# Kernel optimization log

Hardware: AMD Instinct MI355X
Metric: run time of the kernel (lower is better)

## Reference

```python
import jax, jax.numpy as jnp
import numpy as np
from jax import lax

BN_EPS = 1e-5


def conv_bn_relu(x, W, g, b, m, v):
    # 3x3 conv, pad=1, stride=1, no bias; then inference-mode BN; then ReLU
    y = lax.conv_general_dilated(x, W, (1, 1), 'SAME',
                                 dimension_numbers=('NCHW', 'OIHW', 'NCHW'))
    scale = g / jnp.sqrt(v + BN_EPS)
    y = y * scale[None, :, None, None] + (b - m * scale)[None, :, None, None]
    return jax.nn.relu(y)


def shifted_windows(y, d, pad_val):
    # y: [n,c,h,w] -> [k*k, n, c, h, w] of all spatial shifts within radius d
    n, c, h, w = y.shape
    yp = jnp.pad(y, ((0, 0), (0, 0), (d, d), (d, d)), constant_values=pad_val)
    k = 2 * d + 1
    return jnp.stack([yp[:, :, i:i + h, j:j + w] for i in range(k) for j in range(k)], axis=0)


def setup_inputs() -> dict:
    key = jax.random.key(0)
    ks = jax.random.split(key, 16)
    n_clip, n, C_in, H, W = 2, 2, 512, 64, 64
    emb_dim, fc_dim, num_class = 256, 128, 124

    def bn_params(k, c):
        k1, k2, k3, k4 = jax.random.split(k, 4)
        return (jax.random.uniform(k1, (c,)) + 0.5,
                jax.random.normal(k2, (c,)) * 0.1,
                jax.random.normal(k3, (c,)) * 0.1,
                jax.random.uniform(k4, (c,)) + 0.5)

    emb_g, emb_b, emb_m, emb_v = bn_params(ks[0], emb_dim)
    emb2_g, emb2_b, emb2_m, emb2_v = bn_params(ks[1], fc_dim)
    return {
        'clip_embs': jax.random.normal(ks[2], (n_clip * n, C_in, H, W), dtype=jnp.float32),
        'clip_num': 2,
        'emb_W': jax.random.normal(ks[3], (emb_dim, C_in, 3, 3), dtype=jnp.float32) * 0.02,
        'emb_g': emb_g, 'emb_b': emb_b, 'emb_m': emb_m, 'emb_v': emb_v,
        'emb2_W': jax.random.normal(ks[4], (fc_dim, C_in, 3, 3), dtype=jnp.float32) * 0.02,
        'emb2_g': emb2_g, 'emb2_b': emb2_b, 'emb2_m': emb2_m, 'emb2_v': emb2_v,
        'last_W': jax.random.normal(ks[5], (num_class, emb_dim, 1, 1), dtype=jnp.float32) * 0.05,
        'last_b': jnp.zeros((num_class,), dtype=jnp.float32),
    }


MAX_DISTANCES = (2,)
TEMP = 1.0


def reference(clip_embs, clip_num, emb_W, emb_g, emb_b, emb_m, emb_v,
              emb2_W, emb2_g, emb2_b, emb2_m, emb2_v, last_W, last_b):
    # emb_2 features used for the local cost volume (fc_dim channels)
    clip_emb2 = conv_bn_relu(clip_embs, emb2_W, emb2_g, emb2_b, emb2_m, emb2_v)
    chunks2 = jnp.split(clip_emb2, clip_num, axis=0)
    c2 = chunks2[-1]                      # current frame, [n, fc_dim, h, w]
    others2 = chunks2[:-1]

    x2 = jnp.sum(c2 * c2, axis=1)         # [n,h,w]

    all_weights = []                       # per other clip: per max_distance softmax weights
    for other in others2:
        y2 = jnp.sum(other * other, axis=1, keepdims=True)  # [n,1,h,w]
        w_list = []
        for d in MAX_DISTANCES:
            k = 2 * d + 1
            y_sh = shifted_windows(other, d, 0.0)            # [k2,n,c,h,w]
            y2_sh = shifted_windows(y2, d, 1e20)[:, :, 0]    # [k2,n,h,w]
            cross = jnp.einsum('nchw,onchw->onhw', c2, y_sh)
            dist = x2[None] + y2_sh - 2.0 * cross            # [k2,n,h,w] squared L2
            # distsoftmax branch: softmax over the k*k window of 1/(dist*temp+1e-5)
            w_ = jax.nn.softmax(1.0 / (dist * TEMP + 1e-5), axis=0)
            w_list.append(w_)
        all_weights.append(w_list)

    # emb features (emb_dim channels) that get warped
    clip_emb_s = conv_bn_relu(clip_embs, emb_W, emb_g, emb_b, emb_m, emb_v)
    chunks_s = jnp.split(clip_emb_s, clip_num, axis=0)
    c_img = chunks_s[-1]                   # [n, emb_dim, h, w]
    others_s = chunks_s[:-1]

    final_emb = [c_img]
    for other, w_list in zip(others_s, all_weights):
        warp_fs = []
        for d, w_ in zip(MAX_DISTANCES, w_list):
            k = 2 * d + 1
            o_sh = shifted_windows(other, d, 0.0)            # [k2,n,c,h,w]
            # weighted sum over window, then avgpool over k*k -> divide by k*k
            warp = jnp.einsum('onchw,onhw->nchw', o_sh, w_) / (k * k)
            warp_fs.append(warp)
        final_emb.append(jnp.mean(jnp.stack(warp_fs, axis=-1), axis=-1))

    # linear_combine=False: mean over the clip embeddings
    final_fea = jnp.mean(jnp.stack(final_emb, axis=-1), axis=-1)

    # last_layer: dropout (eval -> identity) + 1x1 conv
    logits = jnp.einsum('nchw,oc->nohw', final_fea, last_W[:, :, 0, 0]) + last_b[None, :, None, None]
    x = jax.nn.log_softmax(logits, axis=1)
    return (x, clip_emb2)
```

## Files before the change

### kernel.cpp

```cpp
#include <hip/hip_runtime.h>
#include <hip/hip_bf16.h>
#include <stdint.h>


typedef float v4f __attribute__((ext_vector_type(4)));
typedef __bf16 v8bf __attribute__((ext_vector_type(8)));
typedef unsigned short u16;
typedef unsigned int u32;
typedef u16 u16x8 __attribute__((ext_vector_type(8)));

constexpr size_t XH_OFF  = 0;
constexpr size_t XH_BYTES = (size_t)4*66*66*512*2;
constexpr size_t WT_OFF  = XH_OFF + XH_BYTES;
constexpr size_t WT_BYTES = (size_t)9*384*512*2;
constexpr size_t FS_OFF  = WT_OFF + WT_BYTES;
constexpr size_t FS_BYTES = (size_t)4*68*68*256*2;
constexpr size_t F2_OFF  = FS_OFF + FS_BYTES;
constexpr size_t F2_BYTES = (size_t)4*68*68*128*4;
constexpr size_t Y2_OFF  = F2_OFF + F2_BYTES;
constexpr size_t Y2_BYTES = (size_t)2*68*68*4;
constexpr size_t FEA_OFF = Y2_OFF + Y2_BYTES;
constexpr size_t FEA_BYTES = (size_t)2*4096*256*2;
constexpr size_t WL_OFF  = FEA_OFF + FEA_BYTES;
constexpr size_t WL_BYTES = (size_t)128*256*2;
constexpr size_t SC_OFF  = WL_OFF + WL_BYTES;
constexpr size_t WS_TOTAL = SC_OFF + 768*4;

__device__ __forceinline__ float bf2f(u16 h) { return __uint_as_float(((u32)h) << 16); }
__device__ __forceinline__ u16 f2bf(float f) {
  u32 u = __float_as_uint(f);
  return (u16)((u + 0x7fffu + ((u >> 16) & 1u)) >> 16);
}

__device__ __forceinline__ void gld16(const void* g, const void* l) {
  __builtin_amdgcn_global_load_lds(
      (const __attribute__((address_space(1))) void*)(uintptr_t)g,
      (__attribute__((address_space(3))) void*)(u32)(uintptr_t)l,
      16, 0, 0);
}

__global__ void k_init(const float* __restrict__ eg, const float* __restrict__ eb,
                       const float* __restrict__ em, const float* __restrict__ ev,
                       const float* __restrict__ e2g, const float* __restrict__ e2b,
                       const float* __restrict__ e2m, const float* __restrict__ e2v,
                       const float* __restrict__ lw,
                       u16* __restrict__ Xh, u16* __restrict__ Fs, float* __restrict__ F2,
                       float* __restrict__ Y2, u16* __restrict__ Wl,
                       float* __restrict__ sc, float* __restrict__ bi) {
  const u32 N0 = 4u * 260u * 64u;
  const u32 N1 = 4u * 528u * 32u;
  const u32 N2 = 4u * 528u * 32u;
  const u32 N3 = 2u * 68u * 68u;
  const u32 N4 = 4096u;
  const u32 N5 = 384u;
  const u32 TOT = N0 + N1 + N2 + N3 + N4 + N5;
  const u16x8 z8 = {0,0,0,0,0,0,0,0};
  for (u32 i = blockIdx.x * 256u + threadIdx.x; i < TOT; i += gridDim.x * 256u) {
    if (i < N0) {
      const u32 img = i / (260u * 64u);
      const u32 rem = i - img * (260u * 64u);
      const u32 r = rem >> 6, ch8 = rem & 63u;
      u32 prow, pcol;
      if (r < 132u) { prow = (r >= 66u) ? 65u : 0u; pcol = r - ((r >= 66u) ? 66u : 0u); }
      else { const u32 rr = r - 132u; prow = 1u + (rr >> 1); pcol = (rr & 1u) * 65u; }
      *(u16x8*)(Xh + ((size_t)((img * 66u + prow) * 66u + pcol)) * 512u + ch8 * 8u) = z8;
    } else if (i < N0 + N1 + N2) {
      const bool isF2 = (i >= N0 + N1);
      const u32 j = isF2 ? (i - N0 - N1) : (i - N0);
      const u32 img = j / (528u * 32u);
      const u32 rem = j - img * (528u * 32u);
      const u32 r = rem >> 5, cg = rem & 31u;
      u32 prow, pcol;
      if (r < 272u) { const u32 q = r / 68u; prow = (q < 2u) ? q : q + 64u; pcol = r - q * 68u; }
      else { const u32 rr = r - 272u; prow = 2u + (rr >> 2); const u32 c = rr & 3u; pcol = (c < 2u) ? c : c + 64u; }
      if (isF2) {
        const float4 zf = {0.f, 0.f, 0.f, 0.f};
        *(float4*)(F2 + ((size_t)((img * 68u + prow) * 68u + pcol)) * 128u + cg * 4u) = zf;
      } else {
        *(u16x8*)(Fs + ((size_t)((img * 68u + prow) * 68u + pcol)) * 256u + cg * 8u) = z8;
      }
    } else if (i < N0 + N1 + N2 + N3) {
      const u32 j = i - N0 - N1 - N2;
      const u32 n = j / 4624u, rc = j - n * 4624u;
      const u32 rr = rc / 68u, cc = rc - rr * 68u;
      const bool interior = (rr >= 2u && rr < 66u && cc >= 2u && cc < 66u);
      Y2[j] = interior ? 0.f : 1e20f;
    } else if (i < N0 + N1 + N2 + N3 + N4) {
      const u32 j = i - N0 - N1 - N2 - N3;
      const u32 row = j >> 5, c8 = (j & 31u) * 8u;
      u16x8 o;
      #pragma unroll
      for (int k = 0; k < 8; ++k) o[k] = (row < 124u) ? f2bf(lw[row * 256u + c8 + k]) : (u16)0;
      *(u16x8*)(Wl + (size_t)row * 256u + c8) = o;
    } else {
      const u32 id = i - N0 - N1 - N2 - N3 - N4;
      float g, b, m, v;
      if (id < 256u) { g = eg[id]; b = eb[id]; m = em[id]; v = ev[id]; }
      else { const u32 q = id - 256u; g = e2g[q]; b = e2b[q]; m = e2m[q]; v = e2v[q]; }
      const float s = g / sqrtf(v + 1e-5f);
      sc[id] = s;
      bi[id] = b - m * s;
    }
  }
}

__global__ __launch_bounds__(256) void k_prep_x(const float* __restrict__ X, u16* __restrict__ Xh) {
  __shared__ __align__(16) float tile[64 * 65];
  const int tid = threadIdx.x;
  const int n = blockIdx.x >> 7;
  const int rem = blockIdx.x & 127;
  const int h = rem >> 1, chalf = rem & 1;
  const int wq = tid >> 6, wcol = tid & 63;
  #pragma unroll 1
  for (int it = 0; it < 4; ++it) {
    const int c0 = chalf * 256 + it * 64;
    __syncthreads();
    #pragma unroll
    for (int i = 0; i < 16; ++i) {
      const int cl = i * 4 + wq;
      tile[cl * 65 + wcol] = X[((size_t)(n * 512 + c0 + cl)) * 4096 + h * 64 + wcol];
    }
    __syncthreads();
    const int w = tid >> 2, cg = tid & 3;
    u16x8 a, b;
    #pragma unroll
    for (int j = 0; j < 8; ++j) a[j] = f2bf(tile[(cg * 16 + j) * 65 + w]);
    #pragma unroll
    for (int j = 0; j < 8; ++j) b[j] = f2bf(tile[(cg * 16 + 8 + j) * 65 + w]);
    u16* dst = Xh + ((size_t)((n * 66 + h + 1) * 66 + (w + 1))) * 512 + c0 + cg * 16;
    *(u16x8*)dst = a;
    *((u16x8*)dst + 1) = b;
  }
}

__global__ __launch_bounds__(256) void k_prep_w(const float* __restrict__ embW, const float* __restrict__ emb2W,
                                                u16* __restrict__ Wt) {
  __shared__ float row[4608];
  const int oc = blockIdx.x;
  const int tid = threadIdx.x;
  const float* src = (oc < 256) ? (embW + (size_t)oc * 4608) : (emb2W + (size_t)(oc - 256) * 4608);
  for (int i = tid; i < 4608; i += 256) row[i] = src[i];
  __syncthreads();
  #pragma unroll
  for (int pos = 0; pos < 9; ++pos) {
    const u32 pk = (u32)f2bf(row[(2 * tid) * 9 + pos]) | ((u32)f2bf(row[(2 * tid + 1) * 9 + pos]) << 16);
    *(u32*)(Wt + ((size_t)(pos * 384 + oc)) * 512 + 2 * tid) = pk;
  }
}

__global__ __launch_bounds__(256) void k_conv(const u16* __restrict__ Xh, const u16* __restrict__ Wt,
                                              const float* __restrict__ sc, const float* __restrict__ bi,
                                              float* __restrict__ out2, float* __restrict__ F2,
                                              u16* __restrict__ Fs, float* __restrict__ Y2) {
  __shared__ __align__(16) char lds[42496];
  const int tid = threadIdx.x;
  const int wvi = tid >> 6, lane = tid & 63;
  const int octile = blockIdx.x >> 7;
  const int rest = blockIdx.x & 127;
  const int n = rest >> 5, pt = rest & 31;
  const int h0 = pt * 2;
  const int oc0 = octile * 64;
  const int pxrow = wvi >> 1;
  const int pxc0 = (wvi & 1) * 32;

  float* scl = (float*)(lds + 41984);
  float* bil = scl + 64;
  if (tid < 64) { scl[tid] = sc[oc0 + tid]; bil[tid] = bi[oc0 + tid]; }

  const int arow = tid >> 2;
  const size_t asrc0 = (size_t)(oc0 + arow) * 512 + (((tid & 3) ^ (arow & 3)) << 3);
  const u16* xbase = Xh + (size_t)n * 66 * 66 * 512;
  int bofs[5];
  #pragma unroll
  for (int k = 0; k < 5; ++k) {
    const int idx = k * 256 + tid;
    if (idx < 1056) {
      const int col = idx >> 2;
      const int ssrc = (idx & 3) ^ (col & 3);
      const int imgrow = col / 66, c = col - imgrow * 66;
      bofs[k] = ((h0 + imgrow) * 66 + c) * 512 + ssrc * 8;
    } else bofs[k] = 0;
  }

  auto stageA = [&](int pos, int cc, int buf) {
    gld16(Wt + (size_t)pos * 384 * 512 + asrc0 + cc * 32, lds + buf * 4096 + wvi * 1024);
  };
  auto stageB = [&](int cc, int buf) {
    char* base = lds + 8192 + buf * 16896;
    #pragma unroll
    for (int k = 0; k < 4; ++k)
      gld16(xbase + bofs[k] + cc * 32, base + k * 4096 + wvi * 1024);
    if (tid < 32) gld16(xbase + bofs[4] + cc * 32, base + 16384);
  };

  v4f acc[4][2];
  #pragma unroll
  for (int mt = 0; mt < 4; ++mt) { acc[mt][0] = (v4f){0,0,0,0}; acc[mt][1] = (v4f){0,0,0,0}; }

  int bA = 0, bB = 0;
  stageB(0, 0);
  stageA(0, 0, 0);
  __syncthreads();

  #pragma unroll 1
  for (int cc = 0; cc < 16; ++cc) {
    #pragma unroll
    for (int pos = 0; pos < 9; ++pos) {
      const int ky = pos / 3, kx = pos % 3;
      if (pos < 8) {
        stageA(pos + 1, cc, bA ^ 1);
      } else if (cc < 15) {
        stageB(cc + 1, bB ^ 1);
        stageA(0, cc + 1, bA ^ 1);
      }
      v8bf af[4], bfr[2];
      const char* pA = lds + bA * 4096 + ((lane & 15) << 6) + ((((lane >> 4) ^ (lane & 3))) << 4);
      #pragma unroll
      for (int mt = 0; mt < 4; ++mt) af[mt] = *(const v8bf*)(pA + mt * 1024);
      #pragma unroll
      for (int nt = 0; nt < 2; ++nt) {
        const int rb = (pxrow + ky) * 66 + pxc0 + nt * 16 + (lane & 15) + kx;
        bfr[nt] = *(const v8bf*)(lds + 8192 + bB * 16896 + (rb << 6) + (((lane >> 4) ^ (rb & 3)) << 4));
      }
      #pragma unroll
      for (int mt = 0; mt < 4; ++mt)
        #pragma unroll
        for (int nt = 0; nt < 2; ++nt)
          acc[mt][nt] = __builtin_amdgcn_mfma_f32_16x16x32_bf16(af[mt], bfr[nt], acc[mt][nt], 0, 0, 0);
      __syncthreads();
      bA ^= 1;
      if (pos == 8) bB ^= 1;
    }
  }

  float vals[4][2][4];
  #pragma unroll
  for (int mt = 0; mt < 4; ++mt) {
    const int ocb = mt * 16 + ((lane >> 4) << 2);
    #pragma unroll
    for (int j = 0; j < 4; ++j) {
      const float s = scl[ocb + j], tt = bil[ocb + j];
      #pragma unroll
      for (int nt = 0; nt < 2; ++nt) vals[mt][nt][j] = fmaxf(fmaf(acc[mt][nt][j], s, tt), 0.f);
    }
  }

  if (octile >= 4) {
    #pragma unroll
    for (int mt = 0; mt < 4; ++mt)
      #pragma unroll
      for (int j = 0; j < 4; ++j) {
        const int oc = (octile - 4) * 64 + mt * 16 + ((lane >> 4) << 2) + j;
        float* orow = out2 + ((size_t)(n * 128 + oc)) * 4096 + (h0 + pxrow) * 64 + pxc0;
        orow[(lane & 15)] = vals[mt][0][j];
        orow[16 + (lane & 15)] = vals[mt][1][j];
      }
    if (n < 2) {
      #pragma unroll
      for (int nt = 0; nt < 2; ++nt) {
        float s = 0.f;
        #pragma unroll
        for (int mt = 0; mt < 4; ++mt)
          #pragma unroll
          for (int j = 0; j < 4; ++j) s = fmaf(vals[mt][nt][j], vals[mt][nt][j], s);
        s += __shfl_xor(s, 16);
        s += __shfl_xor(s, 32);
        if ((lane >> 4) == 0)
          atomicAdd(&Y2[(size_t)(n * 68 + h0 + pxrow + 2) * 68 + pxc0 + nt * 16 + (lane & 15) + 2], s);
      }
    }
    float* T = (float*)lds;
    #pragma unroll
    for (int mt = 0; mt < 4; ++mt)
      #pragma unroll
      for (int nt = 0; nt < 2; ++nt)
        #pragma unroll
        for (int j = 0; j < 4; ++j)
          T[(wvi * 32 + nt * 16 + (lane & 15)) * 64 + mt * 16 + ((lane >> 4) << 2) + j] = vals[mt][nt][j];
    __syncthreads();
    const int px = tid >> 1, half = tid & 1;
    const float4* Tp = (const float4*)(T + px * 64 + half * 32);
    float4* dst = (float4*)(F2 + ((size_t)((n * 68 + h0 + (px >> 6) + 2) * 68 + (px & 63) + 2)) * 128 + (octile - 4) * 64 + half * 32);
    #pragma unroll
    for (int i = 0; i < 8; ++i) dst[i] = Tp[i];
  } else {
    u16* T = (u16*)lds;
    #pragma unroll
    for (int mt = 0; mt < 4; ++mt)
      #pragma unroll
      for (int nt = 0; nt < 2; ++nt)
        #pragma unroll
        for (int jj = 0; jj < 2; ++jj) {
          const u32 pk = (u32)f2bf(vals[mt][nt][2 * jj]) | ((u32)f2bf(vals[mt][nt][2 * jj + 1]) << 16);
          *(u32*)(T + (wvi * 32 + nt * 16 + (lane & 15)) * 64 + mt * 16 + ((lane >> 4) << 2) + 2 * jj) = pk;
        }
    __syncthreads();
    const int px = tid >> 1, half = tid & 1;
    const u16x8* Tp = (const u16x8*)(T + px * 64 + half * 32);
    u16x8* dst = (u16x8*)(Fs + ((size_t)((n * 68 + h0 + (px >> 6) + 2) * 68 + (px & 63) + 2)) * 256 + octile * 64 + half * 32);
    #pragma unroll
    for (int i = 0; i < 4; ++i) dst[i] = Tp[i];
  }
}

__global__ __launch_bounds__(256) void k_dw(const float* __restrict__ F2, const float* __restrict__ Y2,
                                            const u16* __restrict__ Fs, u16* __restrict__ Fea) {
  const int t = blockIdx.x * 256 + threadIdx.x;
  const int g = t & 7;
  const int px = t >> 3;
  const int n = px >> 12;
  const int p = px & 4095;
  const int h = p >> 6, w = p & 63;

  const float4* c2p = (const float4*)(F2 + ((size_t)(((n + 2) * 68 + h + 2) * 68 + (w + 2))) * 128 + g * 16);
  float4 c2v[4];
  float x2 = 0.f;
  #pragma unroll
  for (int i = 0; i < 4; ++i) {
    c2v[i] = c2p[i];
    x2 += c2v[i].x * c2v[i].x + c2v[i].y * c2v[i].y + c2v[i].z * c2v[i].z + c2v[i].w * c2v[i].w;
  }
  float cross[25];
  #pragma unroll
  for (int dy = 0; dy < 5; ++dy) {
    const float* rowp = F2 + ((size_t)((n * 68 + h + dy) * 68 + w)) * 128 + g * 16;
    #pragma unroll
    for (int dx = 0; dx < 5; ++dx) {
      const float4* wp = (const float4*)(rowp + dx * 128);
      float s = 0.f;
      #pragma unroll
      for (int i = 0; i < 4; ++i) {
        const float4 u = wp[i];
        s += c2v[i].x * u.x + c2v[i].y * u.y + c2v[i].z * u.z + c2v[i].w * u.w;
      }
      cross[dy * 5 + dx] = s;
    }
  }
  x2 += __shfl_xor(x2, 1); x2 += __shfl_xor(x2, 2); x2 += __shfl_xor(x2, 4);
  #pragma unroll
  for (int o = 0; o < 25; ++o) {
    cross[o] += __shfl_xor(cross[o], 1);
    cross[o] += __shfl_xor(cross[o], 2);
    cross[o] += __shfl_xor(cross[o], 4);
  }
  float wv[25], mx = -1e30f;
  #pragma unroll
  for (int dy = 0; dy < 5; ++dy)
    #pragma unroll
    for (int dx = 0; dx < 5; ++dx) {
      const int o = dy * 5 + dx;
      const float y2v = Y2[(size_t)(n * 68 + h + dy) * 68 + (w + dx)];
      const float dist = x2 + y2v - 2.f * cross[o];
      const float l = 1.f / (dist + 1e-5f);
      wv[o] = l;
      mx = fmaxf(mx, l);
    }
  float ssum = 0.f;
  #pragma unroll
  for (int o = 0; o < 25; ++o) { const float e = __expf(wv[o] - mx); wv[o] = e; ssum += e; }
  const float inv = 1.f / ssum;
  #pragma unroll
  for (int o = 0; o < 25; ++o) wv[o] *= inv;

  float facc[32];
  #pragma unroll
  for (int i = 0; i < 32; ++i) facc[i] = 0.f;
  #pragma unroll
  for (int dy = 0; dy < 5; ++dy) {
    const u16* rp = Fs + ((size_t)((n * 68 + h + dy) * 68 + w)) * 256 + g * 32;
    #pragma unroll
    for (int dx = 0; dx < 5; ++dx) {
      const float wt = wv[dy * 5 + dx];
      const u16x8* up = (const u16x8*)(rp + dx * 256);
      #pragma unroll
      for (int k = 0; k < 4; ++k) {
        const u16x8 u = up[k];
        #pragma unroll
        for (int j = 0; j < 8; ++j) facc[k * 8 + j] = fmaf(wt, bf2f(u[j]), facc[k * 8 + j]);
      }
    }
  }
  const u16x8* cip = (const u16x8*)(Fs + ((size_t)(((n + 2) * 68 + h + 2) * 68 + (w + 2))) * 256 + g * 32);
  u16x8* dp = (u16x8*)(Fea + ((size_t)(n * 4096 + p)) * 256 + g * 32);
  #pragma unroll
  for (int k = 0; k < 4; ++k) {
    const u16x8 cu = cip[k];
    u16x8 ou;
    #pragma unroll
    for (int j = 0; j < 8; ++j)
      ou[j] = f2bf(0.5f * (bf2f(cu[j]) + facc[k * 8 + j] * (1.f / 25.f)));
    dp[k] = ou;
  }
}

__global__ __launch_bounds__(128) void k_logits(const u16* __restrict__ Fea, const u16* __restrict__ Wl,
                                                const float* __restrict__ lb, float* __restrict__ xout) {
  const int wvi = threadIdx.x >> 6, lane = threadIdx.x & 63;
  const int wid = blockIdx.x * 2 + wvi;
  const int n = wid >> 8;
  const int p0 = (wid & 255) * 16;
  const int lp = lane & 15;
  const int kb = (lane >> 4) * 8;

  v4f acc[8];
  #pragma unroll
  for (int mt = 0; mt < 8; ++mt) acc[mt] = (v4f){0.f, 0.f, 0.f, 0.f};

  #pragma unroll
  for (int kc = 0; kc < 8; ++kc) {
    const v8bf b = *(const v8bf*)(Fea + ((size_t)(n * 4096 + p0 + lp)) * 256 + kc * 32 + kb);
    #pragma unroll
    for (int mt = 0; mt < 8; ++mt) {
      const v8bf a = *(const v8bf*)(Wl + ((size_t)(mt * 16 + lp)) * 256 + kc * 32 + kb);
      acc[mt] = __builtin_amdgcn_mfma_f32_16x16x32_bf16(a, b, acc[mt], 0, 0, 0);
    }
  }
  const int r0 = (lane >> 4) * 4;
  float v[8][4];
  float mx = -1e30f;
  #pragma unroll
  for (int mt = 0; mt < 8; ++mt)
    #pragma unroll
    for (int j = 0; j < 4; ++j) {
      const int cls = mt * 16 + r0 + j;
      const float val = (cls < 124) ? (acc[mt][j] + lb[cls]) : -1e30f;
      v[mt][j] = val;
      mx = fmaxf(mx, val);
    }
  mx = fmaxf(mx, __shfl_xor(mx, 16));
  mx = fmaxf(mx, __shfl_xor(mx, 32));
  float s = 0.f;
  #pragma unroll
  for (int mt = 0; mt < 8; ++mt)
    #pragma unroll
    for (int j = 0; j < 4; ++j) {
      const int cls = mt * 16 + r0 + j;
      if (cls < 124) s += __expf(v[mt][j] - mx);
    }
  s += __shfl_xor(s, 16);
  s += __shfl_xor(s, 32);
  const float lz = mx + logf(s);
  #pragma unroll
  for (int mt = 0; mt < 8; ++mt)
    #pragma unroll
    for (int j = 0; j < 4; ++j) {
      const int cls = mt * 16 + r0 + j;
      if (cls < 124)
        xout[((size_t)(n * 124 + cls)) * 4096 + p0 + lp] = v[mt][j] - lz;
    }
}

extern "C" void kernel_launch(void* const* d_in, const int* in_sizes, int n_in,
                              void* d_out, int out_size, void* d_ws, size_t ws_size,
                              hipStream_t stream) {
  (void)in_sizes; (void)n_in; (void)out_size;
  const float* clip  = (const float*)d_in[0];
  const float* embW  = (const float*)d_in[2];
  const float* eg    = (const float*)d_in[3];
  const float* eb    = (const float*)d_in[4];
  const float* em    = (const float*)d_in[5];
  const float* ev    = (const float*)d_in[6];
  const float* emb2W = (const float*)d_in[7];
  const float* e2g   = (const float*)d_in[8];
  const float* e2b   = (const float*)d_in[9];
  const float* e2m   = (const float*)d_in[10];
  const float* e2v   = (const float*)d_in[11];
  const float* lw    = (const float*)d_in[12];
  const float* lb    = (const float*)d_in[13];

  char* ws = (char*)d_ws;
  u16*   Xh  = (u16*)(ws + XH_OFF);
  u16*   Wt  = (u16*)(ws + WT_OFF);
  u16*   Fs  = (u16*)(ws + FS_OFF);
  float* F2  = (float*)(ws + F2_OFF);
  float* Y2  = (float*)(ws + Y2_OFF);
  u16*   Fea = (u16*)(ws + FEA_OFF);
  u16*   Wl  = (u16*)(ws + WL_OFF);
  float* sc  = (float*)(ws + SC_OFF);
  float* bi  = sc + 384;

  float* xout = (float*)d_out;
  float* out2 = xout + (size_t)2 * 124 * 64 * 64;

  if (ws_size < WS_TOTAL) return;

  k_init<<<256, 256, 0, stream>>>(eg, eb, em, ev, e2g, e2b, e2m, e2v, lw, Xh, Fs, F2, Y2, Wl, sc, bi);
  k_prep_x<<<512, 256, 0, stream>>>(clip, Xh);
  k_prep_w<<<384, 256, 0, stream>>>(embW, emb2W, Wt);
  k_conv<<<768, 256, 0, stream>>>(Xh, Wt, sc, bi, out2, F2, Fs, Y2);
  k_dw<<<256, 256, 0, stream>>>(F2, Y2, Fs, Fea);
  k_logits<<<256, 128, 0, stream>>>(Fea, Wl, lb, xout);
}
```

Baseline: 207.7 us.

## Enlarge conv tile to 128 channels with register-direct fragment-layout weights

Weights are pre-packed into an MFMA fragment layout so each wave loads its A operands straight from global memory into registers, prefetched one tap ahead. This removes the A staging through LDS and the per-tap barrier. Each block now computes 128 output channels by 128 pixels, halving the block count and reusing each staged input tile across twice as many channels. The input tile is swizzled differently and the epilogue is reworked. The depthwise warp kernel is also split across twice as many threads with narrower channel groups. In exchange the block uses more accumulator registers and has fewer blocks to hide latency.

Result: slower. 221.5 us (+6.6%).

```diff
diff --git a/kernel.cpp b/kernel.cpp
--- a/kernel.cpp
+++ b/kernel.cpp
@@ -12,7 +12,7 @@
 constexpr size_t XH_OFF  = 0;
 constexpr size_t XH_BYTES = (size_t)4*66*66*512*2;
 constexpr size_t WT_OFF  = XH_OFF + XH_BYTES;
-constexpr size_t WT_BYTES = (size_t)9*384*512*2;
+constexpr size_t WT_BYTES = (size_t)9*16*24*64*8*2;
 constexpr size_t FS_OFF  = WT_OFF + WT_BYTES;
 constexpr size_t FS_BYTES = (size_t)4*68*68*256*2;
 constexpr size_t F2_OFF  = FS_OFF + FS_BYTES;
@@ -134,41 +134,41 @@
 }
 
 __global__ __launch_bounds__(256) void k_prep_w(const float* __restrict__ embW, const float* __restrict__ emb2W,
-                                                u16* __restrict__ Wt) {
+                                                u16* __restrict__ Wf) {
   __shared__ float row[4608];
   const int oc = blockIdx.x;
   const int tid = threadIdx.x;
   const float* src = (oc < 256) ? (embW + (size_t)oc * 4608) : (emb2W + (size_t)(oc - 256) * 4608);
   for (int i = tid; i < 4608; i += 256) row[i] = src[i];
   __syncthreads();
+  const int cc = tid >> 4;
+  const int slot = (tid >> 2) & 3;
+  const int e = 2 * (tid & 3);
+  const int r = oc & 15, ocb = oc >> 4;
   #pragma unroll
   for (int pos = 0; pos < 9; ++pos) {
     const u32 pk = (u32)f2bf(row[(2 * tid) * 9 + pos]) | ((u32)f2bf(row[(2 * tid + 1) * 9 + pos]) << 16);
-    *(u32*)(Wt + ((size_t)(pos * 384 + oc)) * 512 + 2 * tid) = pk;
-  }
-}
-
-__global__ __launch_bounds__(256) void k_conv(const u16* __restrict__ Xh, const u16* __restrict__ Wt,
+    *(u32*)(Wf + ((size_t)((pos * 16 + cc) * 24 + ocb)) * 512 + (slot * 16 + r) * 8 + e) = pk;
+  }
+}
+
+__global__ __launch_bounds__(256) void k_conv(const u16* __restrict__ Xh, const u16* __restrict__ Wf,
                                               const float* __restrict__ sc, const float* __restrict__ bi,
                                               float* __restrict__ out2, float* __restrict__ F2,
                                               u16* __restrict__ Fs, float* __restrict__ Y2) {
-  __shared__ __align__(16) char lds[42496];
+  __shared__ __align__(16) char lds[34816];
   const int tid = threadIdx.x;
   const int wvi = tid >> 6, lane = tid & 63;
   const int octile = blockIdx.x >> 7;
   const int rest = blockIdx.x & 127;
   const int n = rest >> 5, pt = rest & 31;
   const int h0 = pt * 2;
-  const int oc0 = octile * 64;
-  const int pxrow = wvi >> 1;
-  const int pxc0 = (wvi & 1) * 32;
-
-  float* scl = (float*)(lds + 41984);
-  float* bil = scl + 64;
-  if (tid < 64) { scl[tid] = sc[oc0 + tid]; bil[tid] = bi[oc0 + tid]; }
-
-  const int arow = tid >> 2;
-  const size_t asrc0 = (size_t)(oc0 + arow) * 512 + (((tid & 3) ^ (arow & 3)) << 3);
+  const int ochalf = wvi >> 1, prow = wvi & 1;
+
+  float* scl = (float*)(lds + 33792);
+  float* bil = scl + 128;
+  if (tid < 128) { scl[tid] = sc[octile * 128 + tid]; bil[tid] = bi[octile * 128 + tid]; }
+
   const u16* xbase = Xh + (size_t)n * 66 * 66 * 512;
   int bofs[5];
   #pragma unroll
@@ -176,30 +176,42 @@
     const int idx = k * 256 + tid;
     if (idx < 1056) {
       const int col = idx >> 2;
-      const int ssrc = (idx & 3) ^ (col & 3);
+      const int ssrc = (idx & 3) ^ ((col >> 1) & 3);
       const int imgrow = col / 66, c = col - imgrow * 66;
       bofs[k] = ((h0 + imgrow) * 66 + c) * 512 + ssrc * 8;
     } else bofs[k] = 0;
   }
 
-  auto stageA = [&](int pos, int cc, int buf) {
-    gld16(Wt + (size_t)pos * 384 * 512 + asrc0 + cc * 32, lds + buf * 4096 + wvi * 1024);
+  auto stageB = [&](int cc, int buf) {
+    char* base = lds + buf * 16896;
+    #pragma unroll
+    for (int k = 0; k < 4; ++k)
+      gld16(xbase + bofs[k] + cc * 32, base + k * 4096 + tid * 16);
+    if (tid < 32) gld16(xbase + bofs[4] + cc * 32, base + 16384 + tid * 16);
   };
-  auto stageB = [&](int cc, int buf) {
-    char* base = lds + 8192 + buf * 16896;
-    #pragma unroll
-    for (int k = 0; k < 4; ++k)
-      gld16(xbase + bofs[k] + cc * 32, base + k * 4096 + wvi * 1024);
-    if (tid < 32) gld16(xbase + bofs[4] + cc * 32, base + 16384);
+
+  const int ocb0 = octile * 8 + ochalf * 4;
+  const int lane8 = lane * 8;
+  auto loadA = [&](int pos, int cc, int mt) {
+    return *(const v8bf*)(Wf + ((size_t)((pos * 16 + cc) * 24 + ocb0 + mt)) * 512 + lane8);
   };
-
-  v4f acc[4][2];
-  #pragma unroll
-  for (int mt = 0; mt < 4; ++mt) { acc[mt][0] = (v4f){0,0,0,0}; acc[mt][1] = (v4f){0,0,0,0}; }
-
-  int bA = 0, bB = 0;
+  const int rbB = prow * 66 + (lane & 15);
+  const int slotb = lane >> 4;
+  auto readB = [&](int buf, int rb) {
+    return *(const v8bf*)(lds + buf * 16896 + rb * 64 + (((slotb ^ ((rb >> 1) & 3))) << 4));
+  };
+
+  v4f acc[4][4];
+  #pragma unroll
+  for (int mt = 0; mt < 4; ++mt)
+    #pragma unroll
+    for (int nt = 0; nt < 4; ++nt) acc[mt][nt] = (v4f){0.f, 0.f, 0.f, 0.f};
+
+  int buf = 0;
   stageB(0, 0);
-  stageA(0, 0, 0);
+  v8bf ac[4];
+  #pragma unroll
+  for (int mt = 0; mt < 4; ++mt) ac[mt] = loadA(0, 0, mt);
   __syncthreads();
 
   #pragma unroll 1
@@ -207,57 +219,58 @@
     #pragma unroll
     for (int pos = 0; pos < 9; ++pos) {
       const int ky = pos / 3, kx = pos % 3;
+      if (pos == 5 && cc < 15) stageB(cc + 1, buf ^ 1);
+      v8bf an[4];
       if (pos < 8) {
-        stageA(pos + 1, cc, bA ^ 1);
+        #pragma unroll
+        for (int mt = 0; mt < 4; ++mt) an[mt] = loadA(pos + 1, cc, mt);
       } else if (cc < 15) {
-        stageB(cc + 1, bB ^ 1);
-        stageA(0, cc + 1, bA ^ 1);
-      }
-      v8bf af[4], bfr[2];
-      const char* pA = lds + bA * 4096 + ((lane & 15) << 6) + ((((lane >> 4) ^ (lane & 3))) << 4);
-      #pragma unroll
-      for (int mt = 0; mt < 4; ++mt) af[mt] = *(const v8bf*)(pA + mt * 1024);
-      #pragma unroll
-      for (int nt = 0; nt < 2; ++nt) {
-        const int rb = (pxrow + ky) * 66 + pxc0 + nt * 16 + (lane & 15) + kx;
-        bfr[nt] = *(const v8bf*)(lds + 8192 + bB * 16896 + (rb << 6) + (((lane >> 4) ^ (rb & 3)) << 4));
-      }
+        #pragma unroll
+        for (int mt = 0; mt < 4; ++mt) an[mt] = loadA(0, cc + 1, mt);
+      } else {
+        #pragma unroll
+        for (int mt = 0; mt < 4; ++mt) an[mt] = ac[mt];
+      }
+      v8bf bfr[4];
+      #pragma unroll
+      for (int nt = 0; nt < 4; ++nt)
+        bfr[nt] = readB(buf, rbB + ky * 66 + kx + nt * 16);
       #pragma unroll
       for (int mt = 0; mt < 4; ++mt)
         #pragma unroll
-        for (int nt = 0; nt < 2; ++nt)
-          acc[mt][nt] = __builtin_amdgcn_mfma_f32_16x16x32_bf16(af[mt], bfr[nt], acc[mt][nt], 0, 0, 0);
-      __syncthreads();
-      bA ^= 1;
-      if (pos == 8) bB ^= 1;
-    }
-  }
-
-  float vals[4][2][4];
+        for (int nt = 0; nt < 4; ++nt)
+          acc[mt][nt] = __builtin_amdgcn_mfma_f32_16x16x32_bf16(ac[mt], bfr[nt], acc[mt][nt], 0, 0, 0);
+      if (pos == 8) { __syncthreads(); buf ^= 1; }
+      #pragma unroll
+      for (int mt = 0; mt < 4; ++mt) ac[mt] = an[mt];
+    }
+  }
+
+  float vals[4][4][4];
   #pragma unroll
   for (int mt = 0; mt < 4; ++mt) {
-    const int ocb = mt * 16 + ((lane >> 4) << 2);
+    const int ocb = ochalf * 64 + mt * 16 + ((lane >> 4) << 2);
     #pragma unroll
     for (int j = 0; j < 4; ++j) {
       const float s = scl[ocb + j], tt = bil[ocb + j];
       #pragma unroll
-      for (int nt = 0; nt < 2; ++nt) vals[mt][nt][j] = fmaxf(fmaf(acc[mt][nt][j], s, tt), 0.f);
-    }
-  }
-
-  if (octile >= 4) {
+      for (int nt = 0; nt < 4; ++nt) vals[mt][nt][j] = fmaxf(fmaf(acc[mt][nt][j], s, tt), 0.f);
+    }
+  }
+
+  if (octile == 2) {
     #pragma unroll
     for (int mt = 0; mt < 4; ++mt)
       #pragma unroll
       for (int j = 0; j < 4; ++j) {
-        const int oc = (octile - 4) * 64 + mt * 16 + ((lane >> 4) << 2) + j;
-        float* orow = out2 + ((size_t)(n * 128 + oc)) * 4096 + (h0 + pxrow) * 64 + pxc0;
-        orow[(lane & 15)] = vals[mt][0][j];
-        orow[16 + (lane & 15)] = vals[mt][1][j];
+        const int ocl = ochalf * 64 + mt * 16 + ((lane >> 4) << 2) + j;
+        float* orow = out2 + ((size_t)(n * 128 + ocl)) * 4096 + (h0 + prow) * 64;
+        #pragma unroll
+        for (int nt = 0; nt < 4; ++nt) orow[nt * 16 + (lane & 15)] = vals[mt][nt][j];
       }
     if (n < 2) {
       #pragma unroll
-      for (int nt = 0; nt < 2; ++nt) {
+      for (int nt = 0; nt < 4; ++nt) {
         float s = 0.f;
         #pragma unroll
         for (int mt = 0; mt < 4; ++mt)
@@ -266,82 +279,100 @@
         s += __shfl_xor(s, 16);
         s += __shfl_xor(s, 32);
         if ((lane >> 4) == 0)
-          atomicAdd(&Y2[(size_t)(n * 68 + h0 + pxrow + 2) * 68 + pxc0 + nt * 16 + (lane & 15) + 2], s);
+          atomicAdd(&Y2[(size_t)(n * 68 + h0 + prow + 2) * 68 + nt * 16 + (lane & 15) + 2], s);
       }
     }
     float* T = (float*)lds;
-    #pragma unroll
-    for (int mt = 0; mt < 4; ++mt)
-      #pragma unroll
-      for (int nt = 0; nt < 2; ++nt)
-        #pragma unroll
-        for (int j = 0; j < 4; ++j)
-          T[(wvi * 32 + nt * 16 + (lane & 15)) * 64 + mt * 16 + ((lane >> 4) << 2) + j] = vals[mt][nt][j];
-    __syncthreads();
-    const int px = tid >> 1, half = tid & 1;
-    const float4* Tp = (const float4*)(T + px * 64 + half * 32);
-    float4* dst = (float4*)(F2 + ((size_t)((n * 68 + h0 + (px >> 6) + 2) * 68 + (px & 63) + 2)) * 128 + (octile - 4) * 64 + half * 32);
-    #pragma unroll
-    for (int i = 0; i < 8; ++i) dst[i] = Tp[i];
+    #pragma unroll 1
+    for (int mr = 0; mr < 2; ++mr) {
+      __syncthreads();
+      if (ochalf == mr) {
+        #pragma unroll
+        for (int mt = 0; mt < 4; ++mt)
+          #pragma unroll
+          for (int nt = 0; nt < 4; ++nt) {
+            const int p = prow * 64 + nt * 16 + (lane & 15);
+            #pragma unroll
+            for (int j = 0; j < 4; ++j) {
+              const int c = mt * 16 + ((lane >> 4) << 2) + j;
+              T[p * 64 + (((c >> 2) ^ (p & 15)) << 2) + (c & 3)] = vals[mt][nt][j];
+            }
+          }
+      }
+      __syncthreads();
+      const int p = tid >> 1, half = tid & 1;
+      float* dst = F2 + ((size_t)((n * 68 + h0 + (p >> 6) + 2) * 68 + (p & 63) + 2)) * 128 + mr * 64 + half * 32;
+      #pragma unroll
+      for (int i = 0; i < 8; ++i) {
+        const int s = (half * 8 + i) ^ (p & 15);
+        *(float4*)(dst + i * 4) = *(const float4*)(T + p * 64 + s * 4);
+      }
+    }
   } else {
     u16* T = (u16*)lds;
     #pragma unroll
     for (int mt = 0; mt < 4; ++mt)
       #pragma unroll
-      for (int nt = 0; nt < 2; ++nt)
+      for (int nt = 0; nt < 4; ++nt) {
+        const int p = prow * 64 + nt * 16 + (lane & 15);
         #pragma unroll
         for (int jj = 0; jj < 2; ++jj) {
           const u32 pk = (u32)f2bf(vals[mt][nt][2 * jj]) | ((u32)f2bf(vals[mt][nt][2 * jj + 1]) << 16);
-          *(u32*)(T + (wvi * 32 + nt * 16 + (lane & 15)) * 64 + mt * 16 + ((lane >> 4) << 2) + 2 * jj) = pk;
+          const int c = ochalf * 64 + mt * 16 + ((lane >> 4) << 2) + 2 * jj;
+          *(u32*)(T + p * 128 + (((c >> 3) ^ (p & 15)) << 3) + (c & 7)) = pk;
         }
+      }
     __syncthreads();
-    const int px = tid >> 1, half = tid & 1;
-    const u16x8* Tp = (const u16x8*)(T + px * 64 + half * 32);
-    u16x8* dst = (u16x8*)(Fs + ((size_t)((n * 68 + h0 + (px >> 6) + 2) * 68 + (px & 63) + 2)) * 256 + octile * 64 + half * 32);
-    #pragma unroll
-    for (int i = 0; i < 4; ++i) dst[i] = Tp[i];
+    const int p = tid >> 1, half = tid & 1;
+    u16* dst = Fs + ((size_t)((n * 68 + h0 + (p >> 6) + 2) * 68 + (p & 63) + 2)) * 256 + octile * 128 + half * 64;
+    #pragma unroll
+    for (int i = 0; i < 8; ++i) {
+      const int s = (half * 8 + i) ^ (p & 15);
+      *(u16x8*)(dst + i * 8) = *(const u16x8*)(T + p * 128 + s * 8);
+    }
   }
 }
 
 __global__ __launch_bounds__(256) void k_dw(const float* __restrict__ F2, const float* __restrict__ Y2,
                                             const u16* __restrict__ Fs, u16* __restrict__ Fea) {
   const int t = blockIdx.x * 256 + threadIdx.x;
-  const int g = t & 7;
-  const int px = t >> 3;
+  const int g = t & 15;
+  const int px = t >> 4;
   const int n = px >> 12;
   const int p = px & 4095;
   const int h = p >> 6, w = p & 63;
 
-  const float4* c2p = (const float4*)(F2 + ((size_t)(((n + 2) * 68 + h + 2) * 68 + (w + 2))) * 128 + g * 16);
-  float4 c2v[4];
+  const float4* c2p = (const float4*)(F2 + ((size_t)(((n + 2) * 68 + h + 2) * 68 + (w + 2))) * 128 + g * 8);
+  float4 c2v[2];
   float x2 = 0.f;
   #pragma unroll
-  for (int i = 0; i < 4; ++i) {
+  for (int i = 0; i < 2; ++i) {
     c2v[i] = c2p[i];
     x2 += c2v[i].x * c2v[i].x + c2v[i].y * c2v[i].y + c2v[i].z * c2v[i].z + c2v[i].w * c2v[i].w;
   }
   float cross[25];
   #pragma unroll
   for (int dy = 0; dy < 5; ++dy) {
-    const float* rowp = F2 + ((size_t)((n * 68 + h + dy) * 68 + w)) * 128 + g * 16;
+    const float* rowp = F2 + ((size_t)((n * 68 + h + dy) * 68 + w)) * 128 + g * 8;
     #pragma unroll
     for (int dx = 0; dx < 5; ++dx) {
       const float4* wp = (const float4*)(rowp + dx * 128);
       float s = 0.f;
       #pragma unroll
-      for (int i = 0; i < 4; ++i) {
+      for (int i = 0; i < 2; ++i) {
         const float4 u = wp[i];
         s += c2v[i].x * u.x + c2v[i].y * u.y + c2v[i].z * u.z + c2v[i].w * u.w;
       }
       cross[dy * 5 + dx] = s;
     }
   }
-  x2 += __shfl_xor(x2, 1); x2 += __shfl_xor(x2, 2); x2 += __shfl_xor(x2, 4);
+  x2 += __shfl_xor(x2, 1); x2 += __shfl_xor(x2, 2); x2 += __shfl_xor(x2, 4); x2 += __shfl_xor(x2, 8);
   #pragma unroll
   for (int o = 0; o < 25; ++o) {
     cross[o] += __shfl_xor(cross[o], 1);
     cross[o] += __shfl_xor(cross[o], 2);
     cross[o] += __shfl_xor(cross[o], 4);
+    cross[o] += __shfl_xor(cross[o], 8);
   }
   float wv[25], mx = -1e30f;
   #pragma unroll
@@ -362,28 +393,28 @@
   #pragma unroll
   for (int o = 0; o < 25; ++o) wv[o] *= inv;
 
-  float facc[32];
-  #pragma unroll
-  for (int i = 0; i < 32; ++i) facc[i] = 0.f;
+  float facc[16];
+  #pragma unroll
+  for (int i = 0; i < 16; ++i) facc[i] = 0.f;
   #pragma unroll
   for (int dy = 0; dy < 5; ++dy) {
-    const u16* rp = Fs + ((size_t)((n * 68 + h + dy) * 68 + w)) * 256 + g * 32;
+    const u16* rp = Fs + ((size_t)((n * 68 + h + dy) * 68 + w)) * 256 + g * 16;
     #pragma unroll
     for (int dx = 0; dx < 5; ++dx) {
       const float wt = wv[dy * 5 + dx];
       const u16x8* up = (const u16x8*)(rp + dx * 256);
       #pragma unroll
-      for (int k = 0; k < 4; ++k) {
+      for (int k = 0; k < 2; ++k) {
         const u16x8 u = up[k];
         #pragma unroll
         for (int j = 0; j < 8; ++j) facc[k * 8 + j] = fmaf(wt, bf2f(u[j]), facc[k * 8 + j]);
       }
     }
   }
-  const u16x8* cip = (const u16x8*)(Fs + ((size_t)(((n + 2) * 68 + h + 2) * 68 + (w + 2))) * 256 + g * 32);
-  u16x8* dp = (u16x8*)(Fea + ((size_t)(n * 4096 + p)) * 256 + g * 32);
-  #pragma unroll
-  for (int k = 0; k < 4; ++k) {
+  const u16x8* cip = (const u16x8*)(Fs + ((size_t)(((n + 2) * 68 + h + 2) * 68 + (w + 2))) * 256 + g * 16);
+  u16x8* dp = (u16x8*)(Fea + ((size_t)(n * 4096 + p)) * 256 + g * 16);
+  #pragma unroll
+  for (int k = 0; k < 2; ++k) {
     const u16x8 cu = cip[k];
     u16x8 ou;
     #pragma unroll
@@ -470,7 +501,7 @@
 
   char* ws = (char*)d_ws;
   u16*   Xh  = (u16*)(ws + XH_OFF);
-  u16*   Wt  = (u16*)(ws + WT_OFF);
+  u16*   Wf  = (u16*)(ws + WT_OFF);
   u16*   Fs  = (u16*)(ws + FS_OFF);
   float* F2  = (float*)(ws + F2_OFF);
   float* Y2  = (float*)(ws + Y2_OFF);
@@ -486,8 +517,8 @@
 
   k_init<<<256, 256, 0, stream>>>(eg, eb, em, ev, e2g, e2b, e2m, e2v, lw, Xh, Fs, F2, Y2, Wl, sc, bi);
   k_prep_x<<<512, 256, 0, stream>>>(clip, Xh);
-  k_prep_w<<<384, 256, 0, stream>>>(embW, emb2W, Wt);
-  k_conv<<<768, 256, 0, stream>>>(Xh, Wt, sc, bi, out2, F2, Fs, Y2);
-  k_dw<<<256, 256, 0, stream>>>(F2, Y2, Fs, Fea);
+  k_prep_w<<<384, 256, 0, stream>>>(embW, emb2W, Wf);
+  k_conv<<<384, 256, 0, stream>>>(Xh, Wf, sc, bi, out2, F2, Fs, Y2);
+  k_dw<<<512, 256, 0, stream>>>(F2, Y2, Fs, Fea);
   k_logits<<<256, 128, 0, stream>>>(Fea, Wl, lb, xout);
 }
```
